# Kernel tuning notes

Measured on AMD Instinct MI355X. Metric: run time of the kernel, lower is better.

The kernel has to match this reference:

```python
import jax, jax.numpy as jnp
import numpy as np

GAMMA_MIN, GAMMA_MAX = 0.15, 1.0
ALPHA_CAP = 1.0
EPS_L2 = 1e-8
EPS_RMS = 1e-6


def _rmsnorm(x, w):
    return x * jax.lax.rsqrt(jnp.mean(x * x, axis=-1, keepdims=True) + EPS_RMS) * w


def _l2norm(x):
    n = jnp.linalg.norm(x, axis=-1, keepdims=True)
    return x / jnp.maximum(n, EPS_L2)


def _causal_conv(h, kernel):
    # depthwise-shared causal conv over time: out[b,t] = sum_j kernel[j] * h[b, t-j]
    K = kernel.shape[0]
    S = h.shape[1]
    hp = jnp.pad(h, ((0, 0), (K - 1, 0), (0, 0)))
    out = jnp.zeros_like(h)
    for j in range(K):  # K is a small fixed constant (4)
        out = out + kernel[j] * hp[:, K - 1 - j:K - 1 - j + S, :]
    return out


def setup_inputs() -> dict:
    B, S, D, R, K = 8, 1024, 1024, 16, 4
    key = jax.random.key(0)
    ks = jax.random.split(key, 8)
    return {
        'h': jax.random.normal(ks[0], (B, S, D), dtype=jnp.float32),
        'u': jax.random.normal(ks[1], (D, R), dtype=jnp.float32) * 0.05,
        'v': jax.random.normal(ks[2], (D, R), dtype=jnp.float32) * 0.05,
        'decay_logit': jnp.zeros((R,), jnp.float32),
        'alpha_logit': jnp.zeros((R,), jnp.float32),
        'k_base_gate_logit': jnp.float32(0.0),
        'k_base_kernel': jax.random.normal(ks[3], (K,), dtype=jnp.float32) * 0.05,
        'proj_w': jax.random.normal(ks[4], (D, D), dtype=jnp.float32) * 0.02,
        'proj_b': jnp.zeros((D,), jnp.float32),
        'norm1_w': jnp.ones((D,), jnp.float32),
        'norm2_w': jnp.ones((D,), jnp.float32),
        'mlp_w1': jax.random.normal(ks[5], (D, 4 * D), dtype=jnp.float32) * 0.02,
        'mlp_b1': jnp.zeros((4 * D,), jnp.float32),
        'mlp_w2': jax.random.normal(ks[6], (4 * D, D), dtype=jnp.float32) * 0.02,
        'mlp_b2': jnp.zeros((D,), jnp.float32),
    }


def reference(h, u, v, decay_logit, alpha_logit, k_base_gate_logit, k_base_kernel,
              proj_w, proj_b, norm1_w, norm2_w, mlp_w1, mlp_b1, mlp_w2, mlp_b2):
    B, S, D = h.shape
    R = u.shape[1]
    residual = h
    h_norm = _rmsnorm(h, norm1_w)

    # conv k_base term, gated
    gate = jax.nn.sigmoid(k_base_gate_logit)
    out = gate * _causal_conv(h_norm, k_base_kernel)

    # low-rank q/k projections
    alpha = ALPHA_CAP * jax.nn.sigmoid(alpha_logit)  # [R]
    qk = h_norm @ jnp.concatenate((u, v), axis=1)    # [B,S,2R]
    q_raw, k_raw = qk[..., :R], qk[..., R:]
    q = _l2norm(q_raw)
    k = _l2norm(k_raw)

    # per-rank causal decay matrix: w[r,i,j] = gamma[r]^(i-j) for i>=j else 0
    gamma = jnp.clip(jax.nn.sigmoid(decay_logit), GAMMA_MIN, GAMMA_MAX)  # [R]
    pos = jnp.arange(S, dtype=h.dtype)
    diff = jnp.maximum(pos[:, None] - pos[None, :], 0.0)   # [S,S]
    mask = jnp.tril(jnp.ones((S, S), dtype=h.dtype))
    w = (gamma[:, None, None] ** diff) * mask              # [R,S,S]

    q_alpha = q * alpha                                    # [B,S,R]
    A = jnp.einsum('bir,bjr,rij->bij', q_alpha, k, w)      # [B,S,S]
    decay_out = jnp.einsum('bij,bjd->bid', A, h_norm)      # [B,S,D]

    out = out + decay_out
    out = out @ proj_w.T + proj_b
    h2 = residual + out
    hn2 = _rmsnorm(h2, norm2_w)
    mlp_out = jax.nn.gelu(hn2 @ mlp_w1 + mlp_b1) @ mlp_w2 + mlp_b2
    return h2 + mlp_out
```

## Files before the change

kernel.cpp:

```cpp
#include <hip/hip_runtime.h>
#include <hip/hip_bf16.h>
#include <cstdint>
#include <cstddef>

typedef __bf16 bf16;
typedef __bf16 bf16x2 __attribute__((ext_vector_type(2)));
typedef __bf16 bf16x4 __attribute__((ext_vector_type(4)));
typedef __bf16 bf16x8 __attribute__((ext_vector_type(8)));
typedef float  floatx4 __attribute__((ext_vector_type(4)));

#define BB 8
#define SS 1024
#define DD 1024
#define RR 16
#define CHK 64
#define NCH 16

#define PP_ALPHA 0
#define PP_GAMMA 16
#define PP_GP    32
#define PP_KKER  (32 + 16*72)
#define PP_FLOATS 2048

__device__ __forceinline__ float sigmoidf_(float x) { return 1.0f / (1.0f + __expf(-x)); }

__device__ __forceinline__ float gelu_f(float x) {
    float u = 0.7978845608028654f * (x + 0.044715f * x * x * x);
    float t = 1.0f - 2.0f / (__expf(2.0f * u) + 1.0f);
    return 0.5f * x * (1.0f + t);
}

__device__ __forceinline__ void g2l16(const bf16* g, bf16* l) {
    __builtin_amdgcn_global_load_lds(
        (const __attribute__((address_space(1))) void*)g,
        (__attribute__((address_space(3))) void*)l, 16, 0, 0);
}

__global__ void params_kernel(const float* __restrict__ decay_logit,
                              const float* __restrict__ alpha_logit,
                              const float* __restrict__ gate_logit,
                              const float* __restrict__ kbase,
                              float* __restrict__ pp) {
    int t = threadIdx.x;
    if (t < 16) {
        pp[PP_ALPHA + t] = sigmoidf_(alpha_logit[t]);
        float g = sigmoidf_(decay_logit[t]);
        g = fminf(fmaxf(g, 0.15f), 1.0f);
        pp[PP_GAMMA + t] = g;
        float acc = 1.0f;
        for (int p = 0; p < 72; ++p) { pp[PP_GP + t * 72 + p] = acc; acc *= g; }
    }
    if (t >= 16 && t < 20) {
        float gate = sigmoidf_(gate_logit[0]);
        pp[PP_KKER + (t - 16)] = gate * kbase[t - 16];
    }
}

__global__ void uvt_kernel(const float* __restrict__ u, const float* __restrict__ v,
                           bf16* __restrict__ Ut) {
    int c = blockIdx.x;
    const float* src = (c < 16) ? u : v;
    int cc = c & 15;
    for (int d = threadIdx.x; d < 1024; d += 256)
        Ut[c * 1024 + d] = (bf16)src[d * 16 + cc];
}

__global__ __launch_bounds__(256) void rmsqk_kernel(
    const float* __restrict__ h, const bf16* __restrict__ Ut,
    const float* __restrict__ nw, const float* __restrict__ pp,
    bf16* __restrict__ hn, float* __restrict__ qa, float* __restrict__ kk) {
    __shared__ __attribute__((aligned(16))) bf16 Ult[32][1032];
    __shared__ __attribute__((aligned(16))) float hrow[1024];
    __shared__ float red[4];
    __shared__ float qkred[8][32];
    int t = threadIdx.x;
    for (int i = t; i < 32 * 128; i += 256) {
        int c = i >> 7, ch = i & 127;
        *(bf16x8*)&Ult[c][ch * 8] = *(const bf16x8*)(Ut + c * 1024 + ch * 8);
    }
    int lane = t & 63, wid = t >> 6;
    float4 wv = ((const float4*)nw)[t];
    float alpha_t = (t < 16) ? pp[PP_ALPHA + t] : 0.0f;
    size_t row0 = (size_t)blockIdx.x * 16;
    __syncthreads();
    for (int rr = 0; rr < 16; ++rr) {
        size_t row = row0 + rr;
        float4 hv = ((const float4*)(h + row * DD))[t];
        float ss = hv.x*hv.x + hv.y*hv.y + hv.z*hv.z + hv.w*hv.w;
        for (int m = 32; m; m >>= 1) ss += __shfl_xor(ss, m);
        if (lane == 0) red[wid] = ss;
        __syncthreads();
        float tot = red[0] + red[1] + red[2] + red[3];
        float rinv = rsqrtf(tot * (1.0f / 1024.0f) + 1e-6f);
        float x0 = hv.x * rinv * wv.x, x1 = hv.y * rinv * wv.y;
        float x2 = hv.z * rinv * wv.z, x3 = hv.w * rinv * wv.w;
        bf16x4 hb = { (bf16)x0, (bf16)x1, (bf16)x2, (bf16)x3 };
        ((bf16x4*)(hn + row * DD))[t] = hb;
        hrow[t*4+0] = x0; hrow[t*4+1] = x1; hrow[t*4+2] = x2; hrow[t*4+3] = x3;
        __syncthreads();
        int c = t & 31, sg = t >> 5;
        const bf16* up = &Ult[c][sg * 128];
        const float* hp = &hrow[sg * 128];
        float p = 0.0f;
        #pragma unroll
        for (int k8 = 0; k8 < 16; ++k8) {
            bf16x8 u8 = *(const bf16x8*)(up + k8 * 8);
            float4 h0 = *(const float4*)(hp + k8 * 8);
            float4 h1 = *(const float4*)(hp + k8 * 8 + 4);
            p += h0.x*(float)u8[0] + h0.y*(float)u8[1] + h0.z*(float)u8[2] + h0.w*(float)u8[3]
               + h1.x*(float)u8[4] + h1.y*(float)u8[5] + h1.z*(float)u8[6] + h1.w*(float)u8[7];
        }
        qkred[sg][c] = p;
        __syncthreads();
        if (t < 32) {
            float val = 0.0f;
            #pragma unroll
            for (int g = 0; g < 8; ++g) val += qkred[g][t];
            float s2 = val * val;
            s2 += __shfl_xor(s2, 1); s2 += __shfl_xor(s2, 2);
            s2 += __shfl_xor(s2, 4); s2 += __shfl_xor(s2, 8);
            float den = fmaxf(sqrtf(s2), 1e-8f);
            float nvl = val / den;
            if (t < 16) qa[row * RR + t] = nvl * alpha_t;
            else        kk[row * RR + (t - 16)] = nvl;
        }
        __syncthreads();
    }
}

__global__ __launch_bounds__(256) void incr_kernel(
    const bf16* __restrict__ hn, const float* __restrict__ kk,
    const float* __restrict__ pp, float* __restrict__ Inc) {
    __shared__ __attribute__((aligned(16))) float wjr[64][16];
    int t = threadIdx.x;
    int bc = blockIdx.x;
    int d0 = blockIdx.y * 256 + t;
    size_t row0 = (size_t)bc * 64;
    for (int idx = t; idx < 1024; idx += 256) {
        int j = idx >> 4, r = idx & 15;
        wjr[j][r] = kk[(row0 + j) * RR + r] * pp[PP_GP + r * 72 + (63 - j)];
    }
    __syncthreads();
    float acc[16] = {};
    for (int j = 0; j < 64; ++j) {
        float x = (float)hn[(row0 + j) * DD + d0];
        const float4* w4 = (const float4*)wjr[j];
        float4 w0 = w4[0], w1 = w4[1], w2 = w4[2], w3 = w4[3];
        acc[0]  += w0.x * x; acc[1]  += w0.y * x; acc[2]  += w0.z * x; acc[3]  += w0.w * x;
        acc[4]  += w1.x * x; acc[5]  += w1.y * x; acc[6]  += w1.z * x; acc[7]  += w1.w * x;
        acc[8]  += w2.x * x; acc[9]  += w2.y * x; acc[10] += w2.z * x; acc[11] += w2.w * x;
        acc[12] += w3.x * x; acc[13] += w3.y * x; acc[14] += w3.z * x; acc[15] += w3.w * x;
    }
    float* outp = Inc + (size_t)bc * 16 * 1024 + d0;
    #pragma unroll
    for (int r = 0; r < 16; ++r) outp[r * 1024] = acc[r];
}

__global__ __launch_bounds__(256) void scan_kernel(
    const float* __restrict__ Inc, const float* __restrict__ pp,
    float* __restrict__ Sprev) {
    int gid = blockIdx.x * 256 + threadIdx.x;
    int b = gid >> 14, rd = gid & 16383;
    int r = rd >> 10;
    float gd = pp[PP_GP + r * 72 + 64];
    float s = 0.0f;
    for (int c = 0; c < 16; ++c) {
        size_t idx = ((size_t)(b * 16 + c) << 14) + rd;
        Sprev[idx] = s;
        s = s * gd + Inc[idx];
    }
}

__global__ __launch_bounds__(256) void phasec_kernel(
    const bf16* __restrict__ hn, const float* __restrict__ qa, const float* __restrict__ kk,
    const float* __restrict__ Sprev, const float* __restrict__ pp,
    bf16* __restrict__ outpre) {
    __shared__ __attribute__((aligned(16))) float qa_s[64][16];
    __shared__ __attribute__((aligned(16))) float kk_s[64][16];
    __shared__ __attribute__((aligned(16))) float gpt[65][16];
    __shared__ __attribute__((aligned(16))) float Mco[64][80];
    __shared__ __attribute__((aligned(16))) bf16 X[80][256];
    __shared__ __attribute__((aligned(16))) bf16 P3[3][256];
    __shared__ float kks[4];
    int t = threadIdx.x;
    int bc = blockIdx.x;
    int c = bc & 15;
    int dt = blockIdx.y * 256;
    size_t row0 = (size_t)bc * 64;
    for (int idx = t; idx < 1024; idx += 256) {
        int j = idx >> 4, r = idx & 15;
        qa_s[j][r] = qa[(row0 + j) * RR + r];
        kk_s[j][r] = kk[(row0 + j) * RR + r];
    }
    for (int idx = t; idx < 16 * 65; idx += 256) {
        int p = idx >> 4, r = idx & 15;
        gpt[p][r] = pp[PP_GP + r * 72 + p];
    }
    for (int idx = t; idx < 64 * 64; idx += 256) {
        int j = idx >> 6, ch = idx & 63;
        *(bf16x4*)&X[j][ch * 4] = *(const bf16x4*)(hn + (row0 + j) * DD + dt + ch * 4);
    }
    for (int idx = t; idx < 16 * 256; idx += 256) {
        int r = idx >> 8, dd = idx & 255;
        X[64 + r][dd] = (bf16)Sprev[((size_t)bc << 14) + r * 1024 + dt + dd];
    }
    for (int idx = t; idx < 3 * 64; idx += 256) {
        int j = idx >> 6, ch = idx & 63;
        bf16x4 val = {};
        if (c > 0) val = *(const bf16x4*)(hn + (row0 - 3 + j) * DD + dt + ch * 4);
        *(bf16x4*)&P3[j][ch * 4] = val;
    }
    if (t < 4) kks[t] = pp[PP_KKER + t];
    __syncthreads();
    for (int idx = t; idx < 64 * 80; idx += 256) {
        int ii = idx / 80, jj = idx - ii * 80;
        float val;
        if (jj < 64) {
            if (jj <= ii) {
                const float4* qa4 = (const float4*)qa_s[ii];
                const float4* kk4 = (const float4*)kk_s[jj];
                const float4* gp4 = (const float4*)gpt[ii - jj];
                float s = 0.0f;
                #pragma unroll
                for (int x = 0; x < 4; ++x) {
                    float4 qv = qa4[x], kv = kk4[x], gv = gp4[x];
                    s += qv.x*kv.x*gv.x + qv.y*kv.y*gv.y + qv.z*kv.z*gv.z + qv.w*kv.w*gv.w;
                }
                val = s;
            } else val = 0.0f;
        } else {
            int r = jj - 64;
            val = qa_s[ii][r] * gpt[ii + 1][r];
        }
        Mco[ii][jj] = val;
    }
    __syncthreads();
    int g = t >> 6, dd4 = (t & 63) * 4;
    const float* mbase = &Mco[g * 16][0];
    float acc[16][4] = {};
    for (int jc = 0; jc < 20; ++jc) {
        float xv[4][4];
        #pragma unroll
        for (int e = 0; e < 4; ++e) {
            bf16x4 x = *(const bf16x4*)&X[jc * 4 + e][dd4];
            xv[e][0] = (float)x[0]; xv[e][1] = (float)x[1];
            xv[e][2] = (float)x[2]; xv[e][3] = (float)x[3];
        }
        #pragma unroll
        for (int q = 0; q < 16; ++q) {
            float4 m = *(const float4*)(mbase + q * 80 + jc * 4);
            #pragma unroll
            for (int e = 0; e < 4; ++e)
                acc[q][e] += m.x * xv[0][e] + m.y * xv[1][e] + m.z * xv[2][e] + m.w * xv[3][e];
        }
    }
    float k0 = kks[0], k1 = kks[1], k2 = kks[2], k3 = kks[3];
    #pragma unroll
    for (int q = 0; q < 16; ++q) {
        int ii = g * 16 + q;
        const bf16* r0p = &X[ii][dd4];
        const bf16* r1p = (ii >= 1) ? &X[ii - 1][dd4] : &P3[2][dd4];
        const bf16* r2p = (ii >= 2) ? &X[ii - 2][dd4] : &P3[ii + 1][dd4];
        const bf16* r3p = (ii >= 3) ? &X[ii - 3][dd4] : &P3[ii][dd4];
        bf16x4 ob;
        #pragma unroll
        for (int e = 0; e < 4; ++e) {
            float vv = acc[q][e] + k0 * (float)r0p[e] + k1 * (float)r1p[e]
                                 + k2 * (float)r2p[e] + k3 * (float)r3p[e];
            ob[e] = (bf16)vv;
        }
        *(bf16x4*)(outpre + (row0 + ii) * DD + dt + dd4) = ob;
    }
}

__global__ void cvt_bf16_kernel(const float* __restrict__ in, bf16* __restrict__ out, int n4) {
    int i = blockIdx.x * 256 + threadIdx.x;
    if (i < n4) {
        float4 v = ((const float4*)in)[i];
        bf16x4 o = { (bf16)v.x, (bf16)v.y, (bf16)v.z, (bf16)v.w };
        ((bf16x4*)out)[i] = o;
    }
}

__global__ __launch_bounds__(256) void trcvt_kernel(
    const float* __restrict__ in, bf16* __restrict__ out, int K, int N) {
    __shared__ float tl[32][33];
    int x0 = blockIdx.x * 32, y0 = blockIdx.y * 32;
    int tx = threadIdx.x & 31, ty = threadIdx.x >> 5;
    #pragma unroll
    for (int i = 0; i < 4; ++i)
        tl[ty + i * 8][tx] = in[(size_t)(y0 + ty + i * 8) * N + x0 + tx];
    __syncthreads();
    #pragma unroll
    for (int i = 0; i < 4; ++i)
        out[(size_t)(x0 + ty + i * 8) * K + y0 + tx] = (bf16)tl[tx][ty + i * 8];
}

__global__ __launch_bounds__(256) void rms2_kernel(
    const float* __restrict__ h2, const float* __restrict__ nw, bf16* __restrict__ hn2) {
    __shared__ float red[4];
    int t = threadIdx.x;
    size_t row = blockIdx.x;
    float4 hv = ((const float4*)(h2 + row * DD))[t];
    float ss = hv.x*hv.x + hv.y*hv.y + hv.z*hv.z + hv.w*hv.w;
    for (int m = 32; m; m >>= 1) ss += __shfl_xor(ss, m);
    if ((t & 63) == 0) red[t >> 6] = ss;
    __syncthreads();
    float tot = red[0] + red[1] + red[2] + red[3];
    float rinv = rsqrtf(tot * (1.0f / 1024.0f) + 1e-6f);
    float4 wv = ((const float4*)nw)[t];
    bf16x4 o = { (bf16)(hv.x * rinv * wv.x), (bf16)(hv.y * rinv * wv.y),
                 (bf16)(hv.z * rinv * wv.z), (bf16)(hv.w * rinv * wv.w) };
    ((bf16x4*)(hn2 + row * DD))[t] = o;
}

template <int EPI>
__global__ __launch_bounds__(256, 2) void gemm_bt_kernel(
    const bf16* __restrict__ A, const bf16* __restrict__ Bt,
    const float* __restrict__ bias, const float* __restrict__ resid,
    float* __restrict__ outf, bf16* __restrict__ outb, int K, int N) {
    __shared__ __attribute__((aligned(16))) bf16 As[128 * 64];
    __shared__ __attribute__((aligned(16))) bf16 Bs[128 * 64];
    int tid = threadIdx.x, lane = tid & 63, wid = tid >> 6;
    int quad = lane >> 4, l16 = lane & 15;
    int lb = blockIdx.y * gridDim.x + blockIdx.x;
    int xcd = lb & 7, q = lb >> 3;
    int m0 = (xcd * 8 + (q & 7)) * 128;
    int n0 = (q >> 3) * 128;
    int wm = (wid >> 1) * 64, wn = (wid & 1) * 64;
    const bf16* Ap[4]; const bf16* Bp[4]; int lo[4];
    #pragma unroll
    for (int j = 0; j < 4; ++j) {
        int s = j * 256 + tid;
        int row = s >> 3, cc = s & 7;
        int gc = cc ^ (row & 7);
        Ap[j] = A  + (size_t)(m0 + row) * K + gc * 8;
        Bp[j] = Bt + (size_t)(n0 + row) * K + gc * 8;
        lo[j] = s * 8;
    }
    floatx4 acc[4][4] = {};
    for (int kt = 0; kt < K; kt += 64) {
        #pragma unroll
        for (int j = 0; j < 4; ++j) {
            g2l16(Ap[j] + kt, As + lo[j]);
            g2l16(Bp[j] + kt, Bs + lo[j]);
        }
        __syncthreads();
        #pragma unroll
        for (int ks = 0; ks < 2; ++ks) {
            bf16x8 af[4], bfr[4];
            #pragma unroll
            for (int tm = 0; tm < 4; ++tm) {
                int row = wm + tm * 16 + l16;
                int cc = (ks * 4 + quad) ^ (row & 7);
                af[tm] = *(const bf16x8*)(As + row * 64 + cc * 8);
            }
            #pragma unroll
            for (int tn = 0; tn < 4; ++tn) {
                int row = wn + tn * 16 + l16;
                int cc = (ks * 4 + quad) ^ (row & 7);
                bfr[tn] = *(const bf16x8*)(Bs + row * 64 + cc * 8);
            }
            #pragma unroll
            for (int tm = 0; tm < 4; ++tm)
                #pragma unroll
                for (int tn = 0; tn < 4; ++tn)
                    acc[tm][tn] = __builtin_amdgcn_mfma_f32_16x16x32_bf16(
                        af[tm], bfr[tn], acc[tm][tn], 0, 0, 0);
        }
        __syncthreads();
    }
    #pragma unroll
    for (int tn = 0; tn < 4; ++tn) {
        int gn = n0 + wn + tn * 16 + l16;
        float bs = bias[gn];
        #pragma unroll
        for (int tm = 0; tm < 4; ++tm) {
            #pragma unroll
            for (int r = 0; r < 4; ++r) {
                size_t gm = (size_t)m0 + wm + tm * 16 + quad * 4 + r;
                float v = acc[tm][tn][r] + bs;
                if (EPI == 1) {
                    outb[gm * N + gn] = (bf16)gelu_f(v);
                } else {
                    v += resid[gm * N + gn];
                    outf[gm * N + gn] = v;
                }
            }
        }
    }
}

extern "C" void kernel_launch(void* const* d_in, const int* in_sizes, int n_in,
                              void* d_out, int out_size, void* d_ws, size_t ws_size,
                              hipStream_t stream) {
    const float* h           = (const float*)d_in[0];
    const float* u           = (const float*)d_in[1];
    const float* v           = (const float*)d_in[2];
    const float* decay_logit = (const float*)d_in[3];
    const float* alpha_logit = (const float*)d_in[4];
    const float* gate_logit  = (const float*)d_in[5];
    const float* kbase       = (const float*)d_in[6];
    const float* proj_w      = (const float*)d_in[7];
    const float* proj_b      = (const float*)d_in[8];
    const float* norm1_w     = (const float*)d_in[9];
    const float* norm2_w     = (const float*)d_in[10];
    const float* mlp_w1      = (const float*)d_in[11];
    const float* mlp_b1      = (const float*)d_in[12];
    const float* mlp_w2      = (const float*)d_in[13];
    const float* mlp_b2      = (const float*)d_in[14];
    float* out = (float*)d_out;

    char* wsb = (char*)d_ws;
    size_t off = 0;
    auto alloc = [&](size_t bytes) -> void* {
        void* p = wsb + off;
        off += (bytes + 255) & ~(size_t)255;
        return p;
    };
    float* pp     = (float*)alloc(PP_FLOATS * 4);
    bf16*  Ut     = (bf16*) alloc((size_t)32 * 1024 * 2);
    bf16*  hn     = (bf16*) alloc((size_t)8192 * 1024 * 2);
    float* qa     = (float*)alloc((size_t)8192 * 16 * 4);
    float* kk     = (float*)alloc((size_t)8192 * 16 * 4);
    float* Inc    = (float*)alloc((size_t)128 * 16 * 1024 * 4);
    float* Sprev  = (float*)alloc((size_t)128 * 16 * 1024 * 4);
    bf16*  outpre = (bf16*) alloc((size_t)8192 * 1024 * 2);
    float* h2     = (float*)alloc((size_t)8192 * 1024 * 4);
    bf16*  hidden = (bf16*) alloc((size_t)8192 * 4096 * 2);
    bf16*  Wp     = (bf16*) alloc((size_t)1024 * 1024 * 2);
    bf16*  W1t    = (bf16*) alloc((size_t)4096 * 1024 * 2);
    bf16*  W2t    = (bf16*) alloc((size_t)1024 * 4096 * 2);
    bf16*  hn2 = hn;

    params_kernel<<<1, 64, 0, stream>>>(decay_logit, alpha_logit, gate_logit, kbase, pp);
    uvt_kernel<<<32, 256, 0, stream>>>(u, v, Ut);
    cvt_bf16_kernel<<<1024, 256, 0, stream>>>(proj_w, Wp, 1024 * 1024 / 4);
    trcvt_kernel<<<dim3(4096 / 32, 1024 / 32), 256, 0, stream>>>(mlp_w1, W1t, 1024, 4096);
    trcvt_kernel<<<dim3(1024 / 32, 4096 / 32), 256, 0, stream>>>(mlp_w2, W2t, 4096, 1024);
    rmsqk_kernel<<<512, 256, 0, stream>>>(h, Ut, norm1_w, pp, hn, qa, kk);
    incr_kernel<<<dim3(128, 4), 256, 0, stream>>>(hn, kk, pp, Inc);
    scan_kernel<<<512, 256, 0, stream>>>(Inc, pp, Sprev);
    phasec_kernel<<<dim3(128, 4), 256, 0, stream>>>(hn, qa, kk, Sprev, pp, outpre);
    gemm_bt_kernel<0><<<dim3(8, 64), 256, 0, stream>>>(outpre, Wp, proj_b, h, h2, nullptr, 1024, 1024);
    rms2_kernel<<<8192, 256, 0, stream>>>(h2, norm2_w, hn2);
    gemm_bt_kernel<1><<<dim3(32, 64), 256, 0, stream>>>(hn2, W1t, mlp_b1, nullptr, nullptr, hidden, 1024, 4096);
    gemm_bt_kernel<2><<<dim3(8, 64), 256, 0, stream>>>(hidden, W2t, mlp_b2, h2, out, nullptr, 4096, 1024);
}
```

Measured before the change: 431.6 us.

## Move qk projection and chunk output to MFMA and add BK templating to GEMM

The fused per-row RMSNorm plus scalar q/k dot product kernel is split into a generic row RMSNorm kernel and an MFMA-based qk projection GEMM with the L2 normalisation done in its epilogue. The chunk-output kernel now folds the causal conv taps into the coefficient matrix and evaluates everything as one bf16 MFMA matmul over a transposed X tile, using narrower 128-column tiles and twice as many blocks. The GEMM kernel gains a K-tile template parameter, set to 128 for the projection and down-projection GEMMs. This moves scalar FMA work onto matrix cores, at the cost of bf16 rounding of the coefficient matrix, extra launches, and higher LDS use per GEMM block.

```diff
diff --git a/kernel.cpp b/kernel.cpp
--- a/kernel.cpp
+++ b/kernel.cpp
@@ -65,66 +65,97 @@
         Ut[c * 1024 + d] = (bf16)src[d * 16 + cc];
 }
 
-__global__ __launch_bounds__(256) void rmsqk_kernel(
-    const float* __restrict__ h, const bf16* __restrict__ Ut,
-    const float* __restrict__ nw, const float* __restrict__ pp,
-    bf16* __restrict__ hn, float* __restrict__ qa, float* __restrict__ kk) {
-    __shared__ __attribute__((aligned(16))) bf16 Ult[32][1032];
-    __shared__ __attribute__((aligned(16))) float hrow[1024];
+__global__ __launch_bounds__(256) void rmsrow_kernel(
+    const float* __restrict__ x, const float* __restrict__ nw, bf16* __restrict__ y) {
     __shared__ float red[4];
-    __shared__ float qkred[8][32];
     int t = threadIdx.x;
-    for (int i = t; i < 32 * 128; i += 256) {
-        int c = i >> 7, ch = i & 127;
-        *(bf16x8*)&Ult[c][ch * 8] = *(const bf16x8*)(Ut + c * 1024 + ch * 8);
-    }
-    int lane = t & 63, wid = t >> 6;
+    size_t row = blockIdx.x;
+    float4 hv = ((const float4*)(x + row * DD))[t];
+    float ss = hv.x*hv.x + hv.y*hv.y + hv.z*hv.z + hv.w*hv.w;
+    for (int m = 32; m; m >>= 1) ss += __shfl_xor(ss, m);
+    if ((t & 63) == 0) red[t >> 6] = ss;
+    __syncthreads();
+    float tot = red[0] + red[1] + red[2] + red[3];
+    float rinv = rsqrtf(tot * (1.0f / 1024.0f) + 1e-6f);
     float4 wv = ((const float4*)nw)[t];
-    float alpha_t = (t < 16) ? pp[PP_ALPHA + t] : 0.0f;
-    size_t row0 = (size_t)blockIdx.x * 16;
-    __syncthreads();
-    for (int rr = 0; rr < 16; ++rr) {
-        size_t row = row0 + rr;
-        float4 hv = ((const float4*)(h + row * DD))[t];
-        float ss = hv.x*hv.x + hv.y*hv.y + hv.z*hv.z + hv.w*hv.w;
-        for (int m = 32; m; m >>= 1) ss += __shfl_xor(ss, m);
-        if (lane == 0) red[wid] = ss;
+    bf16x4 o = { (bf16)(hv.x * rinv * wv.x), (bf16)(hv.y * rinv * wv.y),
+                 (bf16)(hv.z * rinv * wv.z), (bf16)(hv.w * rinv * wv.w) };
+    ((bf16x4*)(y + row * DD))[t] = o;
+}
+
+__global__ __launch_bounds__(256) void qk_kernel(
+    const bf16* __restrict__ hn, const bf16* __restrict__ Ut,
+    const float* __restrict__ pp, float* __restrict__ qa, float* __restrict__ kk) {
+    __shared__ __attribute__((aligned(16))) bf16 As[128 * 64];
+    __shared__ __attribute__((aligned(16))) bf16 Bs[32 * 64];
+    int tid = threadIdx.x, lane = tid & 63, wid = tid >> 6;
+    int quad = lane >> 4, l16 = lane & 15;
+    int m0 = blockIdx.x * 128;
+    int wm = wid * 32;
+    const bf16* Ap[4]; int lo[4];
+    #pragma unroll
+    for (int j = 0; j < 4; ++j) {
+        int s = j * 256 + tid;
+        int row = s >> 3, cc = s & 7;
+        int gc = cc ^ (row & 7);
+        Ap[j] = hn + (size_t)(m0 + row) * DD + gc * 8;
+        lo[j] = s * 8;
+    }
+    int bs_row = tid >> 3, bs_cc = tid & 7;
+    int bs_gc = bs_cc ^ (bs_row & 7);
+    const bf16* Bp = Ut + (size_t)bs_row * DD + bs_gc * 8;
+    int blo = tid * 8;
+    floatx4 acc[2][2] = {};
+    for (int kt = 0; kt < 1024; kt += 64) {
+        #pragma unroll
+        for (int j = 0; j < 4; ++j) g2l16(Ap[j] + kt, As + lo[j]);
+        g2l16(Bp + kt, Bs + blo);
         __syncthreads();
-        float tot = red[0] + red[1] + red[2] + red[3];
-        float rinv = rsqrtf(tot * (1.0f / 1024.0f) + 1e-6f);
-        float x0 = hv.x * rinv * wv.x, x1 = hv.y * rinv * wv.y;
-        float x2 = hv.z * rinv * wv.z, x3 = hv.w * rinv * wv.w;
-        bf16x4 hb = { (bf16)x0, (bf16)x1, (bf16)x2, (bf16)x3 };
-        ((bf16x4*)(hn + row * DD))[t] = hb;
-        hrow[t*4+0] = x0; hrow[t*4+1] = x1; hrow[t*4+2] = x2; hrow[t*4+3] = x3;
+        #pragma unroll
+        for (int ks = 0; ks < 2; ++ks) {
+            bf16x8 af[2], bfr[2];
+            #pragma unroll
+            for (int tm = 0; tm < 2; ++tm) {
+                int row = wm + tm * 16 + l16;
+                int cc = (ks * 4 + quad) ^ (row & 7);
+                af[tm] = *(const bf16x8*)(As + row * 64 + cc * 8);
+            }
+            #pragma unroll
+            for (int tn = 0; tn < 2; ++tn) {
+                int row = tn * 16 + l16;
+                int cc = (ks * 4 + quad) ^ (row & 7);
+                bfr[tn] = *(const bf16x8*)(Bs + row * 64 + cc * 8);
+            }
+            #pragma unroll
+            for (int tm = 0; tm < 2; ++tm)
+                #pragma unroll
+                for (int tn = 0; tn < 2; ++tn)
+                    acc[tm][tn] = __builtin_amdgcn_mfma_f32_16x16x32_bf16(
+                        af[tm], bfr[tn], acc[tm][tn], 0, 0, 0);
+        }
         __syncthreads();
-        int c = t & 31, sg = t >> 5;
-        const bf16* up = &Ult[c][sg * 128];
-        const float* hp = &hrow[sg * 128];
-        float p = 0.0f;
-        #pragma unroll
-        for (int k8 = 0; k8 < 16; ++k8) {
-            bf16x8 u8 = *(const bf16x8*)(up + k8 * 8);
-            float4 h0 = *(const float4*)(hp + k8 * 8);
-            float4 h1 = *(const float4*)(hp + k8 * 8 + 4);
-            p += h0.x*(float)u8[0] + h0.y*(float)u8[1] + h0.z*(float)u8[2] + h0.w*(float)u8[3]
-               + h1.x*(float)u8[4] + h1.y*(float)u8[5] + h1.z*(float)u8[6] + h1.w*(float)u8[7];
-        }
-        qkred[sg][c] = p;
-        __syncthreads();
-        if (t < 32) {
-            float val = 0.0f;
-            #pragma unroll
-            for (int g = 0; g < 8; ++g) val += qkred[g][t];
-            float s2 = val * val;
-            s2 += __shfl_xor(s2, 1); s2 += __shfl_xor(s2, 2);
-            s2 += __shfl_xor(s2, 4); s2 += __shfl_xor(s2, 8);
-            float den = fmaxf(sqrtf(s2), 1e-8f);
-            float nvl = val / den;
-            if (t < 16) qa[row * RR + t] = nvl * alpha_t;
-            else        kk[row * RR + (t - 16)] = nvl;
-        }
-        __syncthreads();
+    }
+    float alf = pp[PP_ALPHA + l16];
+    #pragma unroll
+    for (int tm = 0; tm < 2; ++tm) {
+        #pragma unroll
+        for (int tn = 0; tn < 2; ++tn) {
+            float s2[4];
+            #pragma unroll
+            for (int r = 0; r < 4; ++r) s2[r] = acc[tm][tn][r] * acc[tm][tn][r];
+            #pragma unroll
+            for (int m = 1; m <= 8; m <<= 1)
+                #pragma unroll
+                for (int r = 0; r < 4; ++r) s2[r] += __shfl_xor(s2[r], m);
+            #pragma unroll
+            for (int r = 0; r < 4; ++r) {
+                size_t row = m0 + wm + tm * 16 + quad * 4 + r;
+                float den = fmaxf(sqrtf(s2[r]), 1e-8f);
+                float nvl = acc[tm][tn][r] / den;
+                if (tn == 0) qa[row * RR + l16] = nvl * alf;
+                else         kk[row * RR + l16] = nvl;
+            }
+        }
     }
 }
 
@@ -171,21 +202,21 @@
     }
 }
 
-__global__ __launch_bounds__(256) void phasec_kernel(
+#define XK 104
+__global__ __launch_bounds__(256, 2) void phasec_kernel(
     const bf16* __restrict__ hn, const float* __restrict__ qa, const float* __restrict__ kk,
     const float* __restrict__ Sprev, const float* __restrict__ pp,
     bf16* __restrict__ outpre) {
+    __shared__ __attribute__((aligned(16))) bf16 Xt[128][XK];
+    __shared__ __attribute__((aligned(16))) bf16 Mb[64][XK];
     __shared__ __attribute__((aligned(16))) float qa_s[64][16];
     __shared__ __attribute__((aligned(16))) float kk_s[64][16];
     __shared__ __attribute__((aligned(16))) float gpt[65][16];
-    __shared__ __attribute__((aligned(16))) float Mco[64][80];
-    __shared__ __attribute__((aligned(16))) bf16 X[80][256];
-    __shared__ __attribute__((aligned(16))) bf16 P3[3][256];
     __shared__ float kks[4];
     int t = threadIdx.x;
     int bc = blockIdx.x;
     int c = bc & 15;
-    int dt = blockIdx.y * 256;
+    int dt = blockIdx.y * 128;
     size_t row0 = (size_t)bc * 64;
     for (int idx = t; idx < 1024; idx += 256) {
         int j = idx >> 4, r = idx & 15;
@@ -196,25 +227,27 @@
         int p = idx >> 4, r = idx & 15;
         gpt[p][r] = pp[PP_GP + r * 72 + p];
     }
-    for (int idx = t; idx < 64 * 64; idx += 256) {
-        int j = idx >> 6, ch = idx & 63;
-        *(bf16x4*)&X[j][ch * 4] = *(const bf16x4*)(hn + (row0 + j) * DD + dt + ch * 4);
-    }
-    for (int idx = t; idx < 16 * 256; idx += 256) {
-        int r = idx >> 8, dd = idx & 255;
-        X[64 + r][dd] = (bf16)Sprev[((size_t)bc << 14) + r * 1024 + dt + dd];
-    }
-    for (int idx = t; idx < 3 * 64; idx += 256) {
-        int j = idx >> 6, ch = idx & 63;
-        bf16x4 val = {};
-        if (c > 0) val = *(const bf16x4*)(hn + (row0 - 3 + j) * DD + dt + ch * 4);
-        *(bf16x4*)&P3[j][ch * 4] = val;
-    }
     if (t < 4) kks[t] = pp[PP_KKER + t];
+    for (int idx = t; idx < 64 * 32; idx += 256) {
+        int j = idx >> 5, ch = idx & 31;
+        bf16x4 hv = *(const bf16x4*)(hn + (row0 + j) * DD + dt + ch * 4);
+        #pragma unroll
+        for (int e = 0; e < 4; ++e) Xt[ch * 4 + e][j] = hv[e];
+    }
+    for (int idx = t; idx < 16 * 128; idx += 256) {
+        int r = idx >> 7, dd = idx & 127;
+        Xt[dd][64 + r] = (bf16)Sprev[((size_t)bc << 14) + r * 1024 + dt + dd];
+    }
+    for (int idx = t; idx < 128 * 16; idx += 256) {
+        int dd = idx >> 4, p = idx & 15;
+        bf16 val = (bf16)0.0f;
+        if (p < 3 && c > 0) val = hn[(row0 - 3 + p) * DD + dt + dd];
+        Xt[dd][80 + p] = val;
+    }
     __syncthreads();
-    for (int idx = t; idx < 64 * 80; idx += 256) {
-        int ii = idx / 80, jj = idx - ii * 80;
-        float val;
+    for (int idx = t; idx < 64 * 96; idx += 256) {
+        int ii = idx / 96, jj = idx - ii * 96;
+        float val = 0.0f;
         if (jj < 64) {
             if (jj <= ii) {
                 const float4* qa4 = (const float4*)qa_s[ii];
@@ -227,49 +260,37 @@
                     s += qv.x*kv.x*gv.x + qv.y*kv.y*gv.y + qv.z*kv.z*gv.z + qv.w*kv.w*gv.w;
                 }
                 val = s;
-            } else val = 0.0f;
-        } else {
+                if (ii - jj <= 3) val += kks[ii - jj];
+            }
+        } else if (jj < 80) {
             int r = jj - 64;
             val = qa_s[ii][r] * gpt[ii + 1][r];
-        }
-        Mco[ii][jj] = val;
+        } else if (jj < 83) {
+            int p = jj - 80;
+            if (ii <= p) val = kks[ii + 3 - p];
+        }
+        Mb[ii][jj] = (bf16)val;
     }
     __syncthreads();
-    int g = t >> 6, dd4 = (t & 63) * 4;
-    const float* mbase = &Mco[g * 16][0];
-    float acc[16][4] = {};
-    for (int jc = 0; jc < 20; ++jc) {
-        float xv[4][4];
-        #pragma unroll
-        for (int e = 0; e < 4; ++e) {
-            bf16x4 x = *(const bf16x4*)&X[jc * 4 + e][dd4];
-            xv[e][0] = (float)x[0]; xv[e][1] = (float)x[1];
-            xv[e][2] = (float)x[2]; xv[e][3] = (float)x[3];
-        }
-        #pragma unroll
-        for (int q = 0; q < 16; ++q) {
-            float4 m = *(const float4*)(mbase + q * 80 + jc * 4);
-            #pragma unroll
-            for (int e = 0; e < 4; ++e)
-                acc[q][e] += m.x * xv[0][e] + m.y * xv[1][e] + m.z * xv[2][e] + m.w * xv[3][e];
-        }
-    }
-    float k0 = kks[0], k1 = kks[1], k2 = kks[2], k3 = kks[3];
-    #pragma unroll
-    for (int q = 0; q < 16; ++q) {
-        int ii = g * 16 + q;
-        const bf16* r0p = &X[ii][dd4];
-        const bf16* r1p = (ii >= 1) ? &X[ii - 1][dd4] : &P3[2][dd4];
-        const bf16* r2p = (ii >= 2) ? &X[ii - 2][dd4] : &P3[ii + 1][dd4];
-        const bf16* r3p = (ii >= 3) ? &X[ii - 3][dd4] : &P3[ii][dd4];
-        bf16x4 ob;
-        #pragma unroll
-        for (int e = 0; e < 4; ++e) {
-            float vv = acc[q][e] + k0 * (float)r0p[e] + k1 * (float)r1p[e]
-                                 + k2 * (float)r2p[e] + k3 * (float)r3p[e];
-            ob[e] = (bf16)vv;
-        }
-        *(bf16x4*)(outpre + (row0 + ii) * DD + dt + dd4) = ob;
+    int lane = t & 63, w = t >> 6;
+    int quad = lane >> 4, l16 = lane & 15;
+    floatx4 acc[8] = {};
+    #pragma unroll
+    for (int ks = 0; ks < 3; ++ks) {
+        bf16x8 af = *(const bf16x8*)(&Mb[w * 16 + l16][ks * 32 + quad * 8]);
+        #pragma unroll
+        for (int tn = 0; tn < 8; ++tn) {
+            bf16x8 bfr = *(const bf16x8*)(&Xt[tn * 16 + l16][ks * 32 + quad * 8]);
+            acc[tn] = __builtin_amdgcn_mfma_f32_16x16x32_bf16(af, bfr, acc[tn], 0, 0, 0);
+        }
+    }
+    #pragma unroll
+    for (int tn = 0; tn < 8; ++tn) {
+        #pragma unroll
+        for (int r = 0; r < 4; ++r) {
+            size_t ii = w * 16 + quad * 4 + r;
+            outpre[(row0 + ii) * DD + dt + tn * 16 + l16] = (bf16)acc[tn][r];
+        }
     }
 }
 
@@ -296,31 +317,15 @@
         out[(size_t)(x0 + ty + i * 8) * K + y0 + tx] = (bf16)tl[tx][ty + i * 8];
 }
 
-__global__ __launch_bounds__(256) void rms2_kernel(
-    const float* __restrict__ h2, const float* __restrict__ nw, bf16* __restrict__ hn2) {
-    __shared__ float red[4];
-    int t = threadIdx.x;
-    size_t row = blockIdx.x;
-    float4 hv = ((const float4*)(h2 + row * DD))[t];
-    float ss = hv.x*hv.x + hv.y*hv.y + hv.z*hv.z + hv.w*hv.w;
-    for (int m = 32; m; m >>= 1) ss += __shfl_xor(ss, m);
-    if ((t & 63) == 0) red[t >> 6] = ss;
-    __syncthreads();
-    float tot = red[0] + red[1] + red[2] + red[3];
-    float rinv = rsqrtf(tot * (1.0f / 1024.0f) + 1e-6f);
-    float4 wv = ((const float4*)nw)[t];
-    bf16x4 o = { (bf16)(hv.x * rinv * wv.x), (bf16)(hv.y * rinv * wv.y),
-                 (bf16)(hv.z * rinv * wv.z), (bf16)(hv.w * rinv * wv.w) };
-    ((bf16x4*)(hn2 + row * DD))[t] = o;
-}
-
-template <int EPI>
+template <int EPI, int BK>
 __global__ __launch_bounds__(256, 2) void gemm_bt_kernel(
     const bf16* __restrict__ A, const bf16* __restrict__ Bt,
     const float* __restrict__ bias, const float* __restrict__ resid,
     float* __restrict__ outf, bf16* __restrict__ outb, int K, int N) {
-    __shared__ __attribute__((aligned(16))) bf16 As[128 * 64];
-    __shared__ __attribute__((aligned(16))) bf16 Bs[128 * 64];
+    constexpr int CH = BK / 8;
+    constexpr int PT = 128 * CH / 256;
+    __shared__ __attribute__((aligned(16))) bf16 As[128 * BK];
+    __shared__ __attribute__((aligned(16))) bf16 Bs[128 * BK];
     int tid = threadIdx.x, lane = tid & 63, wid = tid >> 6;
     int quad = lane >> 4, l16 = lane & 15;
     int lb = blockIdx.y * gridDim.x + blockIdx.x;
@@ -328,38 +333,38 @@
     int m0 = (xcd * 8 + (q & 7)) * 128;
     int n0 = (q >> 3) * 128;
     int wm = (wid >> 1) * 64, wn = (wid & 1) * 64;
-    const bf16* Ap[4]; const bf16* Bp[4]; int lo[4];
-    #pragma unroll
-    for (int j = 0; j < 4; ++j) {
+    const bf16* Ap[PT]; const bf16* Bp[PT]; int lo[PT];
+    #pragma unroll
+    for (int j = 0; j < PT; ++j) {
         int s = j * 256 + tid;
-        int row = s >> 3, cc = s & 7;
-        int gc = cc ^ (row & 7);
+        int row = s / CH, cc = s % CH;
+        int gc = cc ^ (row & (CH - 1));
         Ap[j] = A  + (size_t)(m0 + row) * K + gc * 8;
         Bp[j] = Bt + (size_t)(n0 + row) * K + gc * 8;
         lo[j] = s * 8;
     }
     floatx4 acc[4][4] = {};
-    for (int kt = 0; kt < K; kt += 64) {
-        #pragma unroll
-        for (int j = 0; j < 4; ++j) {
+    for (int kt = 0; kt < K; kt += BK) {
+        #pragma unroll
+        for (int j = 0; j < PT; ++j) {
             g2l16(Ap[j] + kt, As + lo[j]);
             g2l16(Bp[j] + kt, Bs + lo[j]);
         }
         __syncthreads();
         #pragma unroll
-        for (int ks = 0; ks < 2; ++ks) {
+        for (int ks = 0; ks < BK / 32; ++ks) {
             bf16x8 af[4], bfr[4];
             #pragma unroll
             for (int tm = 0; tm < 4; ++tm) {
                 int row = wm + tm * 16 + l16;
-                int cc = (ks * 4 + quad) ^ (row & 7);
-                af[tm] = *(const bf16x8*)(As + row * 64 + cc * 8);
+                int cc = (ks * 4 + quad) ^ (row & (CH - 1));
+                af[tm] = *(const bf16x8*)(As + row * BK + cc * 8);
             }
             #pragma unroll
             for (int tn = 0; tn < 4; ++tn) {
                 int row = wn + tn * 16 + l16;
-                int cc = (ks * 4 + quad) ^ (row & 7);
-                bfr[tn] = *(const bf16x8*)(Bs + row * 64 + cc * 8);
+                int cc = (ks * 4 + quad) ^ (row & (CH - 1));
+                bfr[tn] = *(const bf16x8*)(Bs + row * BK + cc * 8);
             }
             #pragma unroll
             for (int tm = 0; tm < 4; ++tm)
@@ -438,12 +443,13 @@
     cvt_bf16_kernel<<<1024, 256, 0, stream>>>(proj_w, Wp, 1024 * 1024 / 4);
     trcvt_kernel<<<dim3(4096 / 32, 1024 / 32), 256, 0, stream>>>(mlp_w1, W1t, 1024, 4096);
     trcvt_kernel<<<dim3(1024 / 32, 4096 / 32), 256, 0, stream>>>(mlp_w2, W2t, 4096, 1024);
-    rmsqk_kernel<<<512, 256, 0, stream>>>(h, Ut, norm1_w, pp, hn, qa, kk);
+    rmsrow_kernel<<<8192, 256, 0, stream>>>(h, norm1_w, hn);
+    qk_kernel<<<64, 256, 0, stream>>>(hn, Ut, pp, qa, kk);
     incr_kernel<<<dim3(128, 4), 256, 0, stream>>>(hn, kk, pp, Inc);
     scan_kernel<<<512, 256, 0, stream>>>(Inc, pp, Sprev);
-    phasec_kernel<<<dim3(128, 4), 256, 0, stream>>>(hn, qa, kk, Sprev, pp, outpre);
-    gemm_bt_kernel<0><<<dim3(8, 64), 256, 0, stream>>>(outpre, Wp, proj_b, h, h2, nullptr, 1024, 1024);
-    rms2_kernel<<<8192, 256, 0, stream>>>(h2, norm2_w, hn2);
-    gemm_bt_kernel<1><<<dim3(32, 64), 256, 0, stream>>>(hn2, W1t, mlp_b1, nullptr, nullptr, hidden, 1024, 4096);
-    gemm_bt_kernel<2><<<dim3(8, 64), 256, 0, stream>>>(hidden, W2t, mlp_b2, h2, out, nullptr, 4096, 1024);
-}
+    phasec_kernel<<<dim3(128, 8), 256, 0, stream>>>(hn, qa, kk, Sprev, pp, outpre);
+    gemm_bt_kernel<0, 128><<<dim3(8, 64), 256, 0, stream>>>(outpre, Wp, proj_b, h, h2, nullptr, 1024, 1024);
+    rmsrow_kernel<<<8192, 256, 0, stream>>>(h2, norm2_w, hn2);
+    gemm_bt_kernel<1, 64><<<dim3(32, 64), 256, 0, stream>>>(hn2, W1t, mlp_b1, nullptr, nullptr, hidden, 1024, 4096);
+    gemm_bt_kernel<2, 128><<<dim3(8, 64), 256, 0, stream>>>(hidden, W2t, mlp_b2, h2, out, nullptr, 4096, 1024);
+}
```

Measured after the change: 394.1 us. 1.1x faster.
